# Performance work log

Hardware: AMD Instinct MI355X
Metric: run time of the kernel (lower is better)

The kernel has to match this reference:

```python
import jax, jax.numpy as jnp
import numpy as np

N = 100000
E = 1600000
IN_C = 128
HID = 256
K_EIG = 64
OUT_C = 16


def setup_inputs() -> dict:
    key = jax.random.key(0)
    ks = jax.random.split(key, 8)
    x = jax.random.normal(ks[0], (N, IN_C), dtype=jnp.float32)
    edge_index = jax.random.randint(ks[1], (2, E), 0, N)
    MLP_W = jax.random.normal(ks[2], (K_EIG, N), dtype=jnp.float32) * 0.02
    MLP_b = jax.random.normal(ks[3], (K_EIG,), dtype=jnp.float32) * 0.02
    mlpx_W = jax.random.normal(ks[4], (HID, IN_C), dtype=jnp.float32) * 0.05
    mlpx_b = jax.random.normal(ks[5], (HID,), dtype=jnp.float32) * 0.02
    fin_W = jax.random.normal(ks[6], (OUT_C, HID + K_EIG), dtype=jnp.float32) * 0.05
    fin_b = jax.random.normal(ks[7], (OUT_C,), dtype=jnp.float32) * 0.02
    return {"x": x, "edge_index": edge_index, "MLP_W": MLP_W, "MLP_b": MLP_b,
            "mlpx_W": mlpx_W, "mlpx_b": mlpx_b, "fin_W": fin_W, "fin_b": fin_b}


def _spmm(row, col, feats, n):
    # adj is COO with coords (col[e], row[e]) and value 1 -> out[col] += feats[row]
    return jax.ops.segment_sum(feats[row], col, num_segments=n)


def _pump(xA, row, col, n):
    # MinCut-style pump: soft assignment, normalized-cut loss + orthogonality loss
    S = jax.nn.softmax(xA, axis=-1)                      # [N, K]
    AS = _spmm(row, col, S, n)                            # A @ S, [N, K]
    cut = jnp.sum(S * AS)                                 # tr(S^T A S)
    deg = jax.ops.segment_sum(jnp.ones(col.shape, S.dtype), col, num_segments=n)
    deg_term = jnp.sum(deg[:, None] * S * S)              # tr(S^T D S)
    pump_loss = -(cut / deg_term)
    SS = S.T @ S                                          # [K, K]
    k = S.shape[1]
    ortho_loss = jnp.linalg.norm(SS / jnp.linalg.norm(SS)
                                 - jnp.eye(k, dtype=S.dtype) / jnp.sqrt(jnp.asarray(k, S.dtype)))
    return S, pump_loss, ortho_loss


def reference(x, edge_index, MLP_W, MLP_b, mlpx_W, mlpx_b, fin_W, fin_b):
    row, col = edge_index[0], edge_index[1]
    n = x.shape[0]
    # xA = adj @ MLP.weight.T + bias   (irregular gather/scatter over edges)
    xA = _spmm(row, col, MLP_W.T, n) + MLP_b              # [N, K]
    xX = x @ mlpx_W.T + mlpx_b                            # [N, HID]
    xA, pump_loss, ortho_loss = _pump(xA, row, col, n)
    z = jnp.concatenate([xX, xA], axis=1)                 # [N, HID+K]
    # dropout omitted (eval mode)
    z = jax.nn.log_softmax(z @ fin_W.T + fin_b, axis=-1)  # [N, OUT]
    return (z, pump_loss + ortho_loss)
```

## Files before the change

kernel.cpp:

```cpp
#include <hip/hip_runtime.h>
#include <math.h>

#define N_NODES 100000
#define N_EDGES 1600000
#define IN_C    128
#define HID     256
#define KEIG    64
#define OUT_C   16

#define NPB      256
#define NBUCKET  ((N_NODES + NPB - 1) / NPB)
#define EDGE_TILE 4096
#define NTILE    ((N_EDGES + EDGE_TILE - 1) / EDGE_TILE)
#define CAP      7168

#define TRANS_BLOCKS   ((N_NODES + 63) / 64)
#define GATHER_BLOCKS  2048
#define CUT_BLOCKS     2048
#define SSP_BLOCKS     512
#define OUT_BLOCKS     ((N_NODES + 255) / 256)

typedef __attribute__((ext_vector_type(8))) short short8;
typedef __attribute__((ext_vector_type(4))) float f32x4;

__device__ __forceinline__ float wave_sum(float v) {
#pragma unroll
    for (int m = 32; m; m >>= 1) v += __shfl_xor(v, m, 64);
    return v;
}
__device__ __forceinline__ float wave_max(float v) {
#pragma unroll
    for (int m = 32; m; m >>= 1) v = fmaxf(v, __shfl_xor(v, m, 64));
    return v;
}
__device__ __forceinline__ float bf2f(unsigned int u) {
    return __uint_as_float((u & 0xffffu) << 16);
}
__device__ __forceinline__ unsigned short f2bf(float f) {
    unsigned int u = __float_as_uint(f);
    u += 0x7fff + ((u >> 16) & 1);
    return (unsigned short)(u >> 16);
}
__device__ __forceinline__ float fp8tof(int b) {
    return __builtin_amdgcn_cvt_f32_fp8(b, 0);
}
__device__ __forceinline__ unsigned char f2fp8(float f) {
    int p = __builtin_amdgcn_cvt_pk_fp8_f32(f, f, 0, false);
    return (unsigned char)(p & 0xff);
}

#define FMA4(P, s, W) \
    P.x = fmaf(s, W.x, P.x); P.y = fmaf(s, W.y, P.y); \
    P.z = fmaf(s, W.z, P.z); P.w = fmaf(s, W.w, P.w);

__global__ void prep_weff(const float* __restrict__ mlpxW, const float* __restrict__ mlpxb,
                          const float* __restrict__ finW, const float* __restrict__ finb,
                          float* __restrict__ Weff, float* __restrict__ beff,
                          int* __restrict__ bcnt, unsigned char* __restrict__ WT8,
                          unsigned char* __restrict__ S8, int* __restrict__ gpad) {
    int t = blockIdx.x * blockDim.x + threadIdx.x;
    const int NW = (IN_C + KEIG) * OUT_C;
    if (t < NW) {
        int k = t >> 4, o = t & 15;
        float acc;
        if (k < IN_C) {
            acc = 0.f;
            for (int c = 0; c < HID; ++c)
                acc += mlpxW[c * IN_C + k] * finW[o * (HID + KEIG) + c];
        } else {
            acc = finW[o * (HID + KEIG) + HID + (k - IN_C)];
        }
        Weff[k * OUT_C + o] = acc;
    }
    int tb = t - NW;
    if (tb >= 0 && tb < OUT_C) {
        float acc = finb[tb];
        for (int c = 0; c < HID; ++c) acc += mlpxb[c] * finW[tb * (HID + KEIG) + c];
        beff[tb] = acc;
    }
    int tz = t - (NW + OUT_C);
    if (tz >= 0 && tz <= NBUCKET) bcnt[tz] = 0;
    int tp = t - (NW + OUT_C + NBUCKET + 1);
    if (tp >= 0 && tp < 16) {
        ((int*)(WT8 + (size_t)N_NODES * 64))[tp] = 0;
        ((int*)(S8 + (size_t)N_NODES * 64))[tp] = 0;
        if (tp == 0) *gpad = 0;
    }
}

__global__ void transpose_w(const float* __restrict__ W, unsigned char* __restrict__ WT8) {
    __shared__ float tile[64][65];
    int n0 = blockIdx.x * 64;
    int t = threadIdx.x;
    int tn = t & 63, tq = t >> 6;
#pragma unroll
    for (int kk = 0; kk < 16; ++kk) {
        int k = tq * 16 + kk;
        int n = n0 + tn;
        tile[k][tn] = (n < N_NODES) ? W[(long long)k * N_NODES + n] : 0.f;
    }
    __syncthreads();
    int tk = t & 63;
#pragma unroll
    for (int ii = 0; ii < 16; ++ii) {
        int n = n0 + tq * 16 + ii;
        if (n < N_NODES) WT8[(unsigned)n * 64u + tk] = f2fp8(tile[tk][tq * 16 + ii] * 32.f);
    }
}

__global__ void bucket_hist(const int* __restrict__ ei, int* __restrict__ bcnt) {
    __shared__ int h[NBUCKET];
    int t = threadIdx.x;
    for (int i = t; i < NBUCKET; i += 256) h[i] = 0;
    __syncthreads();
    int e0 = blockIdx.x * EDGE_TILE;
    int e1 = min(e0 + EDGE_TILE, N_EDGES);
    for (int e = e0 + t; e < e1; e += 256)
        atomicAdd(&h[ei[N_EDGES + e] >> 8], 1);
    __syncthreads();
    for (int i = t; i < NBUCKET; i += 256)
        if (h[i]) atomicAdd(&bcnt[i], h[i]);
}

__global__ void bucket_scan(const int* __restrict__ bcnt, int* __restrict__ bbase,
                            int* __restrict__ bcur) {
    __shared__ int sh[512];
    int t = threadIdx.x;
    int v = (t < NBUCKET) ? bcnt[t] : 0;
    sh[t] = v;
    __syncthreads();
    for (int d = 1; d < 512; d <<= 1) {
        int u = (t >= d) ? sh[t - d] : 0;
        __syncthreads();
        sh[t] += u;
        __syncthreads();
    }
    if (t < NBUCKET) { bbase[t] = sh[t] - v; bcur[t] = sh[t] - v; }
    if (t == 0) bbase[NBUCKET] = N_EDGES;
}

__global__ void bucket_scatter(const int* __restrict__ ei, int* __restrict__ bcur,
                               int* __restrict__ ebuf) {
    __shared__ int h[NBUCKET];
    __shared__ int gb[NBUCKET];
    __shared__ int lpre[NBUCKET];
    __shared__ int psum[256];
    __shared__ int stage[EDGE_TILE];
    __shared__ short bkt[EDGE_TILE];
    int t = threadIdx.x;
    for (int i = t; i < NBUCKET; i += 256) h[i] = 0;
    __syncthreads();
    int e0 = blockIdx.x * EDGE_TILE;
    int e1 = min(e0 + EDGE_TILE, N_EDGES);
    int nt = e1 - e0;
    for (int e = e0 + t; e < e1; e += 256)
        atomicAdd(&h[ei[N_EDGES + e] >> 8], 1);
    __syncthreads();
    int a0 = (2 * t < NBUCKET) ? h[2 * t] : 0;
    int a1 = (2 * t + 1 < NBUCKET) ? h[2 * t + 1] : 0;
    psum[t] = a0 + a1;
    __syncthreads();
    for (int d = 1; d < 256; d <<= 1) {
        int u = (t >= d) ? psum[t - d] : 0;
        __syncthreads();
        psum[t] += u;
        __syncthreads();
    }
    int base = (t == 0) ? 0 : psum[t - 1];
    if (2 * t < NBUCKET) lpre[2 * t] = base;
    if (2 * t + 1 < NBUCKET) lpre[2 * t + 1] = base + a0;
    __syncthreads();
    for (int i = t; i < NBUCKET; i += 256) {
        int c = h[i];
        gb[i] = c ? atomicAdd(&bcur[i], c) : 0;
        h[i] = lpre[i];
    }
    __syncthreads();
    for (int e = e0 + t; e < e1; e += 256) {
        int r = ei[e];
        int c = ei[N_EDGES + e];
        int b = c >> 8;
        int slot = atomicAdd(&h[b], 1);
        stage[slot] = r | ((c & 255) << 17);
        bkt[slot] = (short)b;
    }
    __syncthreads();
    for (int s = t; s < nt; s += 256) {
        int b = bkt[s];
        ebuf[gb[b] + s - lpre[b]] = stage[s];
    }
}

__global__ void csr_build(const int* __restrict__ ebuf, const int* __restrict__ bbase,
                          int* __restrict__ offsets, int* __restrict__ pstart,
                          int* __restrict__ csr_row, int* __restrict__ gpad) {
    __shared__ int hist[NPB];
    __shared__ int sh[NPB];
    __shared__ int curs[NPB];
    __shared__ int staged[CAP];
    __shared__ int pbase_sh;
    int b = blockIdx.x;
    int t = threadIdx.x;
    int s0 = bbase[b], s1 = bbase[b + 1];
    hist[t] = 0;
    __syncthreads();
    for (int i = s0 + t; i < s1; i += 256)
        atomicAdd(&hist[ebuf[i] >> 17], 1);
    __syncthreads();
    int v = hist[t];
    int pv = (v + 7) & ~7;
    sh[t] = pv;
    __syncthreads();
    for (int d = 1; d < 256; d <<= 1) {
        int u = (t >= d) ? sh[t - d] : 0;
        __syncthreads();
        sh[t] += u;
        __syncthreads();
    }
    int pexcl = sh[t] - pv;
    int pt = sh[255];
    if (t == 0) pbase_sh = atomicAdd(gpad, pt);
    __syncthreads();
    int pbase = pbase_sh;
    int node = b * NPB + t;
    if (node < N_NODES) { offsets[node] = v; pstart[node] = pbase + pexcl; }
    curs[t] = pexcl;
    __syncthreads();
    if (pt <= CAP) {
        for (int i = t; i < pt; i += 256) staged[i] = N_NODES;
        __syncthreads();
        for (int i = s0 + t; i < s1; i += 256) {
            int pk = ebuf[i];
            int pos = atomicAdd(&curs[pk >> 17], 1);
            staged[pos] = pk & 0x1FFFF;
        }
        __syncthreads();
        for (int i = t; i < pt; i += 256) csr_row[pbase + i] = staged[i];
    } else {
        for (int i = t; i < pt; i += 256) csr_row[pbase + i] = N_NODES;
        __syncthreads();
        for (int i = s0 + t; i < s1; i += 256) {
            int pk = ebuf[i];
            int pos = atomicAdd(&curs[pk >> 17], 1);
            csr_row[pbase + pos] = pk & 0x1FFFF;
        }
    }
}

__global__ void gather_softmax(const int* __restrict__ offsets, const int* __restrict__ pstart,
                               const int* __restrict__ csr_row,
                               const unsigned char* __restrict__ WT8,
                               const float* __restrict__ MLPb,
                               unsigned short* __restrict__ Sb,
                               unsigned char* __restrict__ S8,
                               float* __restrict__ dtp) {
    int lane = threadIdx.x & 63;
    int wib = __builtin_amdgcn_readfirstlane(threadIdx.x >> 6);
    int gw = blockIdx.x * 4 + wib;
    int nw = gridDim.x * 4;
    float bias = MLPb[lane];
    float dacc = 0.f;
    for (int n = gw; n < N_NODES; n += nw) {
        int deg = __builtin_amdgcn_readfirstlane(offsets[n]);
        int ps  = __builtin_amdgcn_readfirstlane(pstart[n]);
        int plen = (deg + 7) & ~7;
        float acc = 0.f;
        for (int j = 0; j < plen; j += 8) {
            int r0 = csr_row[ps + j + 0], r1 = csr_row[ps + j + 1];
            int r2 = csr_row[ps + j + 2], r3 = csr_row[ps + j + 3];
            int r4 = csr_row[ps + j + 4], r5 = csr_row[ps + j + 5];
            int r6 = csr_row[ps + j + 6], r7 = csr_row[ps + j + 7];
            int b0 = WT8[(unsigned)r0 * 64u + lane];
            int b1 = WT8[(unsigned)r1 * 64u + lane];
            int b2 = WT8[(unsigned)r2 * 64u + lane];
            int b3 = WT8[(unsigned)r3 * 64u + lane];
            int b4 = WT8[(unsigned)r4 * 64u + lane];
            int b5 = WT8[(unsigned)r5 * 64u + lane];
            int b6 = WT8[(unsigned)r6 * 64u + lane];
            int b7 = WT8[(unsigned)r7 * 64u + lane];
            acc += ((fp8tof(b0) + fp8tof(b1)) + (fp8tof(b2) + fp8tof(b3)))
                 + ((fp8tof(b4) + fp8tof(b5)) + (fp8tof(b6) + fp8tof(b7)));
        }
        acc = bias + acc * 0.03125f;
        float m = wave_max(acc);
        float e = __expf(acc - m);
        float sm = wave_sum(e);
        float sv = e / sm;
        unsigned idx = (unsigned)n * 64u + lane;
        Sb[idx] = f2bf(sv);
        S8[idx] = f2fp8(sv * 64.f);
        dacc += (float)deg * sv * sv;
    }
    dacc = wave_sum(dacc);
    __shared__ float red[4];
    if (lane == 0) red[wib] = dacc;
    __syncthreads();
    if (threadIdx.x == 0) dtp[blockIdx.x] = red[0] + red[1] + red[2] + red[3];
}

__global__ void cut_csr(const int* __restrict__ offsets, const int* __restrict__ pstart,
                        const int* __restrict__ csr_row,
                        const unsigned short* __restrict__ Sb,
                        const unsigned char* __restrict__ S8, float* __restrict__ cutp) {
    int lane = threadIdx.x & 63;
    int wib = __builtin_amdgcn_readfirstlane(threadIdx.x >> 6);
    int gw = blockIdx.x * 4 + wib;
    int nw = gridDim.x * 4;
    float acc = 0.f;
    for (int n = gw; n < N_NODES; n += nw) {
        float sc = bf2f(Sb[(unsigned)n * 64u + lane]);
        int deg = __builtin_amdgcn_readfirstlane(offsets[n]);
        int ps  = __builtin_amdgcn_readfirstlane(pstart[n]);
        int plen = (deg + 7) & ~7;
        float g = 0.f;
        for (int j = 0; j < plen; j += 8) {
            int r0 = csr_row[ps + j + 0], r1 = csr_row[ps + j + 1];
            int r2 = csr_row[ps + j + 2], r3 = csr_row[ps + j + 3];
            int r4 = csr_row[ps + j + 4], r5 = csr_row[ps + j + 5];
            int r6 = csr_row[ps + j + 6], r7 = csr_row[ps + j + 7];
            int b0 = S8[(unsigned)r0 * 64u + lane];
            int b1 = S8[(unsigned)r1 * 64u + lane];
            int b2 = S8[(unsigned)r2 * 64u + lane];
            int b3 = S8[(unsigned)r3 * 64u + lane];
            int b4 = S8[(unsigned)r4 * 64u + lane];
            int b5 = S8[(unsigned)r5 * 64u + lane];
            int b6 = S8[(unsigned)r6 * 64u + lane];
            int b7 = S8[(unsigned)r7 * 64u + lane];
            g += ((fp8tof(b0) + fp8tof(b1)) + (fp8tof(b2) + fp8tof(b3)))
               + ((fp8tof(b4) + fp8tof(b5)) + (fp8tof(b6) + fp8tof(b7)));
        }
        acc += sc * g * 0.015625f;
    }
    acc = wave_sum(acc);
    __shared__ float red[4];
    if (lane == 0) red[wib] = acc;
    __syncthreads();
    if (threadIdx.x == 0) cutp[blockIdx.x] = red[0] + red[1] + red[2] + red[3];
}

__global__ __launch_bounds__(256) void ss_mfma(const unsigned short* __restrict__ Sb,
                                               float* __restrict__ ssp) {
    __shared__ unsigned short Sr[32][66];
    int t = threadIdx.x;
    int lane = t & 63;
    int w = t >> 6;
    int m = lane & 15;
    int quad = lane >> 4;
    int srow = t >> 3;
    int spart = t & 7;

    f32x4 a0 = {0.f,0.f,0.f,0.f}, a1 = {0.f,0.f,0.f,0.f};
    f32x4 a2 = {0.f,0.f,0.f,0.f}, a3 = {0.f,0.f,0.f,0.f};

    for (int base = blockIdx.x * 32; base < N_NODES; base += SSP_BLOCKS * 32) {
        const uint4* g = (const uint4*)(Sb + (long long)(base + srow) * 64 + spart * 8);
        uint4 d = *g;
        __syncthreads();
        unsigned int* rowp = (unsigned int*)&Sr[srow][0];
        rowp[spart * 4 + 0] = d.x;
        rowp[spart * 4 + 1] = d.y;
        rowp[spart * 4 + 2] = d.z;
        rowp[spart * 4 + 3] = d.w;
        __syncthreads();

        short8 f0, f1, f2, f3;
#pragma unroll
        for (int j = 0; j < 8; ++j) {
            int k = quad * 8 + j;
            f0[j] = (short)Sr[k][m];
            f1[j] = (short)Sr[k][16 + m];
            f2[j] = (short)Sr[k][32 + m];
            f3[j] = (short)Sr[k][48 + m];
        }
        short8 fa = (w == 0) ? f0 : (w == 1) ? f1 : (w == 2) ? f2 : f3;
        a0 = __builtin_amdgcn_mfma_f32_16x16x32_bf16(fa, f0, a0, 0, 0, 0);
        a1 = __builtin_amdgcn_mfma_f32_16x16x32_bf16(fa, f1, a1, 0, 0, 0);
        a2 = __builtin_amdgcn_mfma_f32_16x16x32_bf16(fa, f2, a2, 0, 0, 0);
        a3 = __builtin_amdgcn_mfma_f32_16x16x32_bf16(fa, f3, a3, 0, 0, 0);
    }

    float* dst = ssp + (size_t)blockIdx.x * 4096;
#pragma unroll
    for (int r = 0; r < 4; ++r) {
        int row = w * 16 + quad * 4 + r;
        dst[row * 64 +  0 + m] = a0[r];
        dst[row * 64 + 16 + m] = a1[r];
        dst[row * 64 + 32 + m] = a2[r];
        dst[row * 64 + 48 + m] = a3[r];
    }
}

__global__ void reduce_ss(const float* __restrict__ ssp, float* __restrict__ SS) {
    int e = blockIdx.x * blockDim.x + threadIdx.x;
    float s = 0.f;
    for (int p = 0; p < SSP_BLOCKS; ++p) s += ssp[(size_t)p * 4096 + e];
    SS[e] = s;
}

__global__ void scalars_kernel(const float* __restrict__ cutp, const float* __restrict__ dtp,
                               const float* __restrict__ SS, float* __restrict__ out) {
    __shared__ float red[256];
    int t = threadIdx.x;
    float c = 0.f;
    for (int i = t; i < CUT_BLOCKS; i += 256) c += cutp[i];
    red[t] = c; __syncthreads();
    for (int s = 128; s; s >>= 1) { if (t < s) red[t] += red[t + s]; __syncthreads(); }
    float cut = red[0]; __syncthreads();

    float d = 0.f;
    for (int i = t; i < GATHER_BLOCKS; i += 256) d += dtp[i];
    red[t] = d; __syncthreads();
    for (int s = 128; s; s >>= 1) { if (t < s) red[t] += red[t + s]; __syncthreads(); }
    float dterm = red[0]; __syncthreads();

    float ss[16];
    float sq = 0.f;
#pragma unroll
    for (int j = 0; j < 16; ++j) { ss[j] = SS[t * 16 + j]; sq += ss[j] * ss[j]; }
    red[t] = sq; __syncthreads();
    for (int s = 128; s; s >>= 1) { if (t < s) red[t] += red[t + s]; __syncthreads(); }
    float nrm = sqrtf(red[0]); __syncthreads();

    float osq = 0.f;
#pragma unroll
    for (int j = 0; j < 16; ++j) {
        int idx = t * 16 + j;
        float v = ss[j] / nrm - ((idx % 65 == 0) ? 0.125f : 0.f);
        osq += v * v;
    }
    red[t] = osq; __syncthreads();
    for (int s = 128; s; s >>= 1) { if (t < s) red[t] += red[t + s]; __syncthreads(); }
    if (t == 0) {
        float loss = -(cut / dterm) + sqrtf(red[0]);
        out[(long long)N_NODES * OUT_C] = loss;
    }
}

__global__ __launch_bounds__(256) void out_kernel(const float* __restrict__ x,
                           const unsigned short* __restrict__ Sb,
                           const float* __restrict__ Weff, const float* __restrict__ beff,
                           float* __restrict__ out) {
    __shared__ float4 Wsh[192 * 4];
    __shared__ float bsh[16];
    int t = threadIdx.x;
    const float4* W4 = (const float4*)Weff;
    for (int i = t; i < 768; i += 256) Wsh[i] = W4[i];
    if (t < 16) bsh[t] = beff[t];
    __syncthreads();

    int r = blockIdx.x * 256 + t;
    if (r >= N_NODES) return;

    float4 p0 = make_float4(bsh[0], bsh[1], bsh[2], bsh[3]);
    float4 p1 = make_float4(bsh[4], bsh[5], bsh[6], bsh[7]);
    float4 p2 = make_float4(bsh[8], bsh[9], bsh[10], bsh[11]);
    float4 p3 = make_float4(bsh[12], bsh[13], bsh[14], bsh[15]);

    const float4* xr = (const float4*)(x + (long long)r * IN_C);
#pragma unroll 8
    for (int j = 0; j < 32; ++j) {
        float4 xv = xr[j];
        int k = j * 4;
        float xs[4] = {xv.x, xv.y, xv.z, xv.w};
#pragma unroll
        for (int c = 0; c < 4; ++c) {
            float s = xs[c];
            float4 w0 = Wsh[(k + c) * 4 + 0];
            float4 w1 = Wsh[(k + c) * 4 + 1];
            float4 w2 = Wsh[(k + c) * 4 + 2];
            float4 w3 = Wsh[(k + c) * 4 + 3];
            FMA4(p0, s, w0); FMA4(p1, s, w1); FMA4(p2, s, w2); FMA4(p3, s, w3);
        }
    }
    const uint2* sr = (const uint2*)(Sb + (long long)r * 64);
#pragma unroll 8
    for (int j = 0; j < 16; ++j) {
        uint2 u = sr[j];
        float xs[4] = {bf2f(u.x), bf2f(u.x >> 16), bf2f(u.y), bf2f(u.y >> 16)};
        int k = IN_C + j * 4;
#pragma unroll
        for (int c = 0; c < 4; ++c) {
            float s = xs[c];
            float4 w0 = Wsh[(k + c) * 4 + 0];
            float4 w1 = Wsh[(k + c) * 4 + 1];
            float4 w2 = Wsh[(k + c) * 4 + 2];
            float4 w3 = Wsh[(k + c) * 4 + 3];
            FMA4(p0, s, w0); FMA4(p1, s, w1); FMA4(p2, s, w2); FMA4(p3, s, w3);
        }
    }

    float m = fmaxf(fmaxf(fmaxf(p0.x, p0.y), fmaxf(p0.z, p0.w)),
                    fmaxf(fmaxf(fmaxf(p1.x, p1.y), fmaxf(p1.z, p1.w)),
                          fmaxf(fmaxf(fmaxf(p2.x, p2.y), fmaxf(p2.z, p2.w)),
                                fmaxf(fmaxf(p3.x, p3.y), fmaxf(p3.z, p3.w)))));
    float sum = __expf(p0.x - m) + __expf(p0.y - m) + __expf(p0.z - m) + __expf(p0.w - m)
              + __expf(p1.x - m) + __expf(p1.y - m) + __expf(p1.z - m) + __expf(p1.w - m)
              + __expf(p2.x - m) + __expf(p2.y - m) + __expf(p2.z - m) + __expf(p2.w - m)
              + __expf(p3.x - m) + __expf(p3.y - m) + __expf(p3.z - m) + __expf(p3.w - m);
    float lse = m + logf(sum);
    float4* o4 = (float4*)(out + (long long)r * OUT_C);
    o4[0] = make_float4(p0.x - lse, p0.y - lse, p0.z - lse, p0.w - lse);
    o4[1] = make_float4(p1.x - lse, p1.y - lse, p1.z - lse, p1.w - lse);
    o4[2] = make_float4(p2.x - lse, p2.y - lse, p2.z - lse, p2.w - lse);
    o4[3] = make_float4(p3.x - lse, p3.y - lse, p3.z - lse, p3.w - lse);
}

extern "C" void kernel_launch(void* const* d_in, const int* in_sizes, int n_in,
                              void* d_out, int out_size, void* d_ws, size_t ws_size,
                              hipStream_t stream) {
    const float* x     = (const float*)d_in[0];
    const int*   ei    = (const int*)d_in[1];
    const float* MLPW  = (const float*)d_in[2];
    const float* MLPb  = (const float*)d_in[3];
    const float* mlpxW = (const float*)d_in[4];
    const float* mlpxb = (const float*)d_in[5];
    const float* finW  = (const float*)d_in[6];
    const float* finb  = (const float*)d_in[7];
    float* out = (float*)d_out;
    char* ws = (char*)d_ws;

    unsigned char*  WT8 = (unsigned char*)ws;
    unsigned char*  S8  = (unsigned char*)(ws + (size_t)(N_NODES + 1) * 64);
    unsigned short* Sb  = (unsigned short*)(ws + (size_t)(N_NODES + 1) * 128);
    char* p = ws + (size_t)(N_NODES + 1) * 128 + (size_t)N_NODES * 128;
    float* ssp  = (float*)p;
    float* SS   = ssp + (size_t)SSP_BLOCKS * 4096;
    float* Weff = SS + 4096;
    float* beff = Weff + 192 * 16;
    float* cutp = beff + 16;
    float* dtp  = cutp + CUT_BLOCKS;
    int* ebuf    = (int*)(dtp + GATHER_BLOCKS);
    int* csr_row = ebuf + N_EDGES;
    int* offsets = csr_row + N_EDGES + 8 * ((N_NODES + NPB - 1) / NPB) * NPB + 8 * N_NODES;
    int* pstart  = offsets + N_NODES + 1;
    int* bcnt    = pstart + N_NODES;
    int* bbase   = bcnt + NBUCKET + 1;
    int* bcur    = bbase + NBUCKET + 1;
    int* gpad    = bcur + NBUCKET;

    hipLaunchKernelGGL(prep_weff, dim3(16), dim3(256), 0, stream,
                       mlpxW, mlpxb, finW, finb, Weff, beff, bcnt, WT8, S8, gpad);
    hipLaunchKernelGGL(transpose_w, dim3(TRANS_BLOCKS), dim3(256), 0, stream, MLPW, WT8);
    hipLaunchKernelGGL(bucket_hist, dim3(NTILE), dim3(256), 0, stream, ei, bcnt);
    hipLaunchKernelGGL(bucket_scan, dim3(1), dim3(512), 0, stream, bcnt, bbase, bcur);
    hipLaunchKernelGGL(bucket_scatter, dim3(NTILE), dim3(256), 0, stream, ei, bcur, ebuf);
    hipLaunchKernelGGL(csr_build, dim3(NBUCKET), dim3(256), 0, stream,
                       ebuf, bbase, offsets, pstart, csr_row, gpad);
    hipLaunchKernelGGL(gather_softmax, dim3(GATHER_BLOCKS), dim3(256), 0, stream,
                       offsets, pstart, csr_row, WT8, MLPb, Sb, S8, dtp);
    hipLaunchKernelGGL(cut_csr, dim3(CUT_BLOCKS), dim3(256), 0, stream,
                       offsets, pstart, csr_row, Sb, S8, cutp);
    hipLaunchKernelGGL(ss_mfma, dim3(SSP_BLOCKS), dim3(256), 0, stream, Sb, ssp);
    hipLaunchKernelGGL(reduce_ss, dim3(16), dim3(256), 0, stream, ssp, SS);
    hipLaunchKernelGGL(scalars_kernel, dim3(1), dim3(256), 0, stream, cutp, dtp, SS, out);
    hipLaunchKernelGGL(out_kernel, dim3(OUT_BLOCKS), dim3(256), 0, stream, x, Sb, Weff, beff, out);
}
```

Before: 308.5 us.

## Fuse prep and tail kernels by block range, unroll gathers to 16 edges

Merges transpose_w with bucket_hist into one launch, and cut_csr, ss_mfma and out_kernel into one launch, choosing the branch by block index. The aim is to cut launch gaps and let independent work share the GPU. CSR rows are now padded to multiples of 16 and the gather loops unrolled to 16 loads, for more memory parallelism per wave. In exchange, the padding adds extra dummy reads on low-degree nodes, and a larger CAP raises shared memory per block in csr_build.

```diff
diff --git a/kernel.cpp b/kernel.cpp
--- a/kernel.cpp
+++ b/kernel.cpp
@@ -12,13 +12,14 @@
 #define NBUCKET  ((N_NODES + NPB - 1) / NPB)
 #define EDGE_TILE 4096
 #define NTILE    ((N_EDGES + EDGE_TILE - 1) / EDGE_TILE)
-#define CAP      7168
+#define CAP      8960
 
 #define TRANS_BLOCKS   ((N_NODES + 63) / 64)
 #define GATHER_BLOCKS  2048
 #define CUT_BLOCKS     2048
 #define SSP_BLOCKS     512
 #define OUT_BLOCKS     ((N_NODES + 255) / 256)
+#define TAIL_BLOCKS    (CUT_BLOCKS + SSP_BLOCKS + OUT_BLOCKS)
 
 typedef __attribute__((ext_vector_type(8))) short short8;
 typedef __attribute__((ext_vector_type(4))) float f32x4;
@@ -52,6 +53,29 @@
 #define FMA4(P, s, W) \
     P.x = fmaf(s, W.x, P.x); P.y = fmaf(s, W.y, P.y); \
     P.z = fmaf(s, W.z, P.z); P.w = fmaf(s, W.w, P.w);
+
+#define GATHER16(TBL, DST) do {                                               \
+    int r0 = csr_row[ps + j + 0],  r1 = csr_row[ps + j + 1];                  \
+    int r2 = csr_row[ps + j + 2],  r3 = csr_row[ps + j + 3];                  \
+    int r4 = csr_row[ps + j + 4],  r5 = csr_row[ps + j + 5];                  \
+    int r6 = csr_row[ps + j + 6],  r7 = csr_row[ps + j + 7];                  \
+    int r8 = csr_row[ps + j + 8],  r9 = csr_row[ps + j + 9];                  \
+    int rA = csr_row[ps + j + 10], rB = csr_row[ps + j + 11];                 \
+    int rC = csr_row[ps + j + 12], rD = csr_row[ps + j + 13];                 \
+    int rE = csr_row[ps + j + 14], rF = csr_row[ps + j + 15];                 \
+    int b0 = TBL[(unsigned)r0 * 64u + lane], b1 = TBL[(unsigned)r1 * 64u + lane]; \
+    int b2 = TBL[(unsigned)r2 * 64u + lane], b3 = TBL[(unsigned)r3 * 64u + lane]; \
+    int b4 = TBL[(unsigned)r4 * 64u + lane], b5 = TBL[(unsigned)r5 * 64u + lane]; \
+    int b6 = TBL[(unsigned)r6 * 64u + lane], b7 = TBL[(unsigned)r7 * 64u + lane]; \
+    int b8 = TBL[(unsigned)r8 * 64u + lane], b9 = TBL[(unsigned)r9 * 64u + lane]; \
+    int bA = TBL[(unsigned)rA * 64u + lane], bB = TBL[(unsigned)rB * 64u + lane]; \
+    int bC = TBL[(unsigned)rC * 64u + lane], bD = TBL[(unsigned)rD * 64u + lane]; \
+    int bE = TBL[(unsigned)rE * 64u + lane], bF = TBL[(unsigned)rF * 64u + lane]; \
+    DST += (((fp8tof(b0) + fp8tof(b1)) + (fp8tof(b2) + fp8tof(b3)))           \
+          + ((fp8tof(b4) + fp8tof(b5)) + (fp8tof(b6) + fp8tof(b7))))          \
+         + (((fp8tof(b8) + fp8tof(b9)) + (fp8tof(bA) + fp8tof(bB)))           \
+          + ((fp8tof(bC) + fp8tof(bD)) + (fp8tof(bE) + fp8tof(bF))));         \
+} while (0)
 
 __global__ void prep_weff(const float* __restrict__ mlpxW, const float* __restrict__ mlpxb,
                           const float* __restrict__ finW, const float* __restrict__ finb,
@@ -88,38 +112,42 @@
     }
 }
 
-__global__ void transpose_w(const float* __restrict__ W, unsigned char* __restrict__ WT8) {
-    __shared__ float tile[64][65];
-    int n0 = blockIdx.x * 64;
+__global__ __launch_bounds__(256) void fused_prep(const float* __restrict__ W,
+                                                  unsigned char* __restrict__ WT8,
+                                                  const int* __restrict__ ei,
+                                                  int* __restrict__ bcnt) {
+    __shared__ __align__(16) char sm[64 * 65 * 4];
     int t = threadIdx.x;
-    int tn = t & 63, tq = t >> 6;
-#pragma unroll
-    for (int kk = 0; kk < 16; ++kk) {
-        int k = tq * 16 + kk;
-        int n = n0 + tn;
-        tile[k][tn] = (n < N_NODES) ? W[(long long)k * N_NODES + n] : 0.f;
-    }
-    __syncthreads();
-    int tk = t & 63;
-#pragma unroll
-    for (int ii = 0; ii < 16; ++ii) {
-        int n = n0 + tq * 16 + ii;
-        if (n < N_NODES) WT8[(unsigned)n * 64u + tk] = f2fp8(tile[tk][tq * 16 + ii] * 32.f);
-    }
-}
-
-__global__ void bucket_hist(const int* __restrict__ ei, int* __restrict__ bcnt) {
-    __shared__ int h[NBUCKET];
-    int t = threadIdx.x;
-    for (int i = t; i < NBUCKET; i += 256) h[i] = 0;
-    __syncthreads();
-    int e0 = blockIdx.x * EDGE_TILE;
-    int e1 = min(e0 + EDGE_TILE, N_EDGES);
-    for (int e = e0 + t; e < e1; e += 256)
-        atomicAdd(&h[ei[N_EDGES + e] >> 8], 1);
-    __syncthreads();
-    for (int i = t; i < NBUCKET; i += 256)
-        if (h[i]) atomicAdd(&bcnt[i], h[i]);
+    if (blockIdx.x < TRANS_BLOCKS) {
+        float (*tile)[65] = (float (*)[65])sm;
+        int n0 = blockIdx.x * 64;
+        int tn = t & 63, tq = t >> 6;
+#pragma unroll
+        for (int kk = 0; kk < 16; ++kk) {
+            int k = tq * 16 + kk;
+            int n = n0 + tn;
+            tile[k][tn] = (n < N_NODES) ? W[(long long)k * N_NODES + n] : 0.f;
+        }
+        __syncthreads();
+        int tk = t & 63;
+#pragma unroll
+        for (int ii = 0; ii < 16; ++ii) {
+            int n = n0 + tq * 16 + ii;
+            if (n < N_NODES) WT8[(unsigned)n * 64u + tk] = f2fp8(tile[tk][tq * 16 + ii] * 32.f);
+        }
+    } else {
+        int* h = (int*)sm;
+        for (int i = t; i < NBUCKET; i += 256) h[i] = 0;
+        __syncthreads();
+        int tile_i = blockIdx.x - TRANS_BLOCKS;
+        int e0 = tile_i * EDGE_TILE;
+        int e1 = min(e0 + EDGE_TILE, N_EDGES);
+        for (int e = e0 + t; e < e1; e += 256)
+            atomicAdd(&h[ei[N_EDGES + e] >> 8], 1);
+        __syncthreads();
+        for (int i = t; i < NBUCKET; i += 256)
+            if (h[i]) atomicAdd(&bcnt[i], h[i]);
+    }
 }
 
 __global__ void bucket_scan(const int* __restrict__ bcnt, int* __restrict__ bbase,
@@ -208,7 +236,7 @@
         atomicAdd(&hist[ebuf[i] >> 17], 1);
     __syncthreads();
     int v = hist[t];
-    int pv = (v + 7) & ~7;
+    int pv = (v + 15) & ~15;
     sh[t] = pv;
     __syncthreads();
     for (int d = 1; d < 256; d <<= 1) {
@@ -263,24 +291,9 @@
     for (int n = gw; n < N_NODES; n += nw) {
         int deg = __builtin_amdgcn_readfirstlane(offsets[n]);
         int ps  = __builtin_amdgcn_readfirstlane(pstart[n]);
-        int plen = (deg + 7) & ~7;
+        int plen = (deg + 15) & ~15;
         float acc = 0.f;
-        for (int j = 0; j < plen; j += 8) {
-            int r0 = csr_row[ps + j + 0], r1 = csr_row[ps + j + 1];
-            int r2 = csr_row[ps + j + 2], r3 = csr_row[ps + j + 3];
-            int r4 = csr_row[ps + j + 4], r5 = csr_row[ps + j + 5];
-            int r6 = csr_row[ps + j + 6], r7 = csr_row[ps + j + 7];
-            int b0 = WT8[(unsigned)r0 * 64u + lane];
-            int b1 = WT8[(unsigned)r1 * 64u + lane];
-            int b2 = WT8[(unsigned)r2 * 64u + lane];
-            int b3 = WT8[(unsigned)r3 * 64u + lane];
-            int b4 = WT8[(unsigned)r4 * 64u + lane];
-            int b5 = WT8[(unsigned)r5 * 64u + lane];
-            int b6 = WT8[(unsigned)r6 * 64u + lane];
-            int b7 = WT8[(unsigned)r7 * 64u + lane];
-            acc += ((fp8tof(b0) + fp8tof(b1)) + (fp8tof(b2) + fp8tof(b3)))
-                 + ((fp8tof(b4) + fp8tof(b5)) + (fp8tof(b6) + fp8tof(b7)));
-        }
+        for (int j = 0; j < plen; j += 16) GATHER16(WT8, acc);
         acc = bias + acc * 0.03125f;
         float m = wave_max(acc);
         float e = __expf(acc - m);
@@ -298,95 +311,141 @@
     if (threadIdx.x == 0) dtp[blockIdx.x] = red[0] + red[1] + red[2] + red[3];
 }
 
-__global__ void cut_csr(const int* __restrict__ offsets, const int* __restrict__ pstart,
-                        const int* __restrict__ csr_row,
-                        const unsigned short* __restrict__ Sb,
-                        const unsigned char* __restrict__ S8, float* __restrict__ cutp) {
-    int lane = threadIdx.x & 63;
-    int wib = __builtin_amdgcn_readfirstlane(threadIdx.x >> 6);
-    int gw = blockIdx.x * 4 + wib;
-    int nw = gridDim.x * 4;
-    float acc = 0.f;
-    for (int n = gw; n < N_NODES; n += nw) {
-        float sc = bf2f(Sb[(unsigned)n * 64u + lane]);
-        int deg = __builtin_amdgcn_readfirstlane(offsets[n]);
-        int ps  = __builtin_amdgcn_readfirstlane(pstart[n]);
-        int plen = (deg + 7) & ~7;
-        float g = 0.f;
-        for (int j = 0; j < plen; j += 8) {
-            int r0 = csr_row[ps + j + 0], r1 = csr_row[ps + j + 1];
-            int r2 = csr_row[ps + j + 2], r3 = csr_row[ps + j + 3];
-            int r4 = csr_row[ps + j + 4], r5 = csr_row[ps + j + 5];
-            int r6 = csr_row[ps + j + 6], r7 = csr_row[ps + j + 7];
-            int b0 = S8[(unsigned)r0 * 64u + lane];
-            int b1 = S8[(unsigned)r1 * 64u + lane];
-            int b2 = S8[(unsigned)r2 * 64u + lane];
-            int b3 = S8[(unsigned)r3 * 64u + lane];
-            int b4 = S8[(unsigned)r4 * 64u + lane];
-            int b5 = S8[(unsigned)r5 * 64u + lane];
-            int b6 = S8[(unsigned)r6 * 64u + lane];
-            int b7 = S8[(unsigned)r7 * 64u + lane];
-            g += ((fp8tof(b0) + fp8tof(b1)) + (fp8tof(b2) + fp8tof(b3)))
-               + ((fp8tof(b4) + fp8tof(b5)) + (fp8tof(b6) + fp8tof(b7)));
-        }
-        acc += sc * g * 0.015625f;
-    }
-    acc = wave_sum(acc);
-    __shared__ float red[4];
-    if (lane == 0) red[wib] = acc;
-    __syncthreads();
-    if (threadIdx.x == 0) cutp[blockIdx.x] = red[0] + red[1] + red[2] + red[3];
-}
-
-__global__ __launch_bounds__(256) void ss_mfma(const unsigned short* __restrict__ Sb,
-                                               float* __restrict__ ssp) {
-    __shared__ unsigned short Sr[32][66];
+__global__ __launch_bounds__(256) void fused_tail(
+        const int* __restrict__ offsets, const int* __restrict__ pstart,
+        const int* __restrict__ csr_row,
+        const unsigned short* __restrict__ Sb, const unsigned char* __restrict__ S8,
+        float* __restrict__ cutp, float* __restrict__ ssp,
+        const float* __restrict__ x, const float* __restrict__ Weff,
+        const float* __restrict__ beff, float* __restrict__ out) {
+    __shared__ __align__(16) char sm[768 * 16 + 64];
     int t = threadIdx.x;
-    int lane = t & 63;
-    int w = t >> 6;
-    int m = lane & 15;
-    int quad = lane >> 4;
-    int srow = t >> 3;
-    int spart = t & 7;
-
-    f32x4 a0 = {0.f,0.f,0.f,0.f}, a1 = {0.f,0.f,0.f,0.f};
-    f32x4 a2 = {0.f,0.f,0.f,0.f}, a3 = {0.f,0.f,0.f,0.f};
-
-    for (int base = blockIdx.x * 32; base < N_NODES; base += SSP_BLOCKS * 32) {
-        const uint4* g = (const uint4*)(Sb + (long long)(base + srow) * 64 + spart * 8);
-        uint4 d = *g;
-        __syncthreads();
-        unsigned int* rowp = (unsigned int*)&Sr[srow][0];
-        rowp[spart * 4 + 0] = d.x;
-        rowp[spart * 4 + 1] = d.y;
-        rowp[spart * 4 + 2] = d.z;
-        rowp[spart * 4 + 3] = d.w;
-        __syncthreads();
-
-        short8 f0, f1, f2, f3;
-#pragma unroll
-        for (int j = 0; j < 8; ++j) {
-            int k = quad * 8 + j;
-            f0[j] = (short)Sr[k][m];
-            f1[j] = (short)Sr[k][16 + m];
-            f2[j] = (short)Sr[k][32 + m];
-            f3[j] = (short)Sr[k][48 + m];
-        }
-        short8 fa = (w == 0) ? f0 : (w == 1) ? f1 : (w == 2) ? f2 : f3;
-        a0 = __builtin_amdgcn_mfma_f32_16x16x32_bf16(fa, f0, a0, 0, 0, 0);
-        a1 = __builtin_amdgcn_mfma_f32_16x16x32_bf16(fa, f1, a1, 0, 0, 0);
-        a2 = __builtin_amdgcn_mfma_f32_16x16x32_bf16(fa, f2, a2, 0, 0, 0);
-        a3 = __builtin_amdgcn_mfma_f32_16x16x32_bf16(fa, f3, a3, 0, 0, 0);
-    }
-
-    float* dst = ssp + (size_t)blockIdx.x * 4096;
-#pragma unroll
-    for (int r = 0; r < 4; ++r) {
-        int row = w * 16 + quad * 4 + r;
-        dst[row * 64 +  0 + m] = a0[r];
-        dst[row * 64 + 16 + m] = a1[r];
-        dst[row * 64 + 32 + m] = a2[r];
-        dst[row * 64 + 48 + m] = a3[r];
+    int bid = blockIdx.x;
+
+    if (bid < CUT_BLOCKS) {
+        int lane = t & 63;
+        int wib = __builtin_amdgcn_readfirstlane(t >> 6);
+        int gw = bid * 4 + wib;
+        int nw = CUT_BLOCKS * 4;
+        float acc = 0.f;
+        for (int n = gw; n < N_NODES; n += nw) {
+            float sc = bf2f(Sb[(unsigned)n * 64u + lane]);
+            int deg = __builtin_amdgcn_readfirstlane(offsets[n]);
+            int ps  = __builtin_amdgcn_readfirstlane(pstart[n]);
+            int plen = (deg + 15) & ~15;
+            float g = 0.f;
+            for (int j = 0; j < plen; j += 16) GATHER16(S8, g);
+            acc += sc * g * 0.015625f;
+        }
+        acc = wave_sum(acc);
+        float* red = (float*)sm;
+        if (lane == 0) red[wib] = acc;
+        __syncthreads();
+        if (t == 0) cutp[bid] = red[0] + red[1] + red[2] + red[3];
+    } else if (bid < CUT_BLOCKS + SSP_BLOCKS) {
+        int bid2 = bid - CUT_BLOCKS;
+        unsigned short (*Sr)[66] = (unsigned short (*)[66])sm;
+        int lane = t & 63;
+        int w = t >> 6;
+        int m = lane & 15;
+        int quad = lane >> 4;
+        int srow = t >> 3;
+        int spart = t & 7;
+        f32x4 a0 = {0.f,0.f,0.f,0.f}, a1 = {0.f,0.f,0.f,0.f};
+        f32x4 a2 = {0.f,0.f,0.f,0.f}, a3 = {0.f,0.f,0.f,0.f};
+        for (int base = bid2 * 32; base < N_NODES; base += SSP_BLOCKS * 32) {
+            const uint4* g = (const uint4*)(Sb + (long long)(base + srow) * 64 + spart * 8);
+            uint4 d = *g;
+            __syncthreads();
+            unsigned int* rowp = (unsigned int*)&Sr[srow][0];
+            rowp[spart * 4 + 0] = d.x;
+            rowp[spart * 4 + 1] = d.y;
+            rowp[spart * 4 + 2] = d.z;
+            rowp[spart * 4 + 3] = d.w;
+            __syncthreads();
+            short8 f0, f1, f2, f3;
+#pragma unroll
+            for (int j = 0; j < 8; ++j) {
+                int k = quad * 8 + j;
+                f0[j] = (short)Sr[k][m];
+                f1[j] = (short)Sr[k][16 + m];
+                f2[j] = (short)Sr[k][32 + m];
+                f3[j] = (short)Sr[k][48 + m];
+            }
+            short8 fa = (w == 0) ? f0 : (w == 1) ? f1 : (w == 2) ? f2 : f3;
+            a0 = __builtin_amdgcn_mfma_f32_16x16x32_bf16(fa, f0, a0, 0, 0, 0);
+            a1 = __builtin_amdgcn_mfma_f32_16x16x32_bf16(fa, f1, a1, 0, 0, 0);
+            a2 = __builtin_amdgcn_mfma_f32_16x16x32_bf16(fa, f2, a2, 0, 0, 0);
+            a3 = __builtin_amdgcn_mfma_f32_16x16x32_bf16(fa, f3, a3, 0, 0, 0);
+        }
+        float* dst = ssp + (size_t)bid2 * 4096;
+#pragma unroll
+        for (int r = 0; r < 4; ++r) {
+            int row = w * 16 + quad * 4 + r;
+            dst[row * 64 +  0 + m] = a0[r];
+            dst[row * 64 + 16 + m] = a1[r];
+            dst[row * 64 + 32 + m] = a2[r];
+            dst[row * 64 + 48 + m] = a3[r];
+        }
+    } else {
+        float4* Wsh = (float4*)sm;
+        float* bsh = (float*)(sm + 768 * 16);
+        const float4* W4 = (const float4*)Weff;
+        for (int i = t; i < 768; i += 256) Wsh[i] = W4[i];
+        if (t < 16) bsh[t] = beff[t];
+        __syncthreads();
+        int r = (bid - CUT_BLOCKS - SSP_BLOCKS) * 256 + t;
+        if (r >= N_NODES) return;
+        float4 p0 = make_float4(bsh[0], bsh[1], bsh[2], bsh[3]);
+        float4 p1 = make_float4(bsh[4], bsh[5], bsh[6], bsh[7]);
+        float4 p2 = make_float4(bsh[8], bsh[9], bsh[10], bsh[11]);
+        float4 p3 = make_float4(bsh[12], bsh[13], bsh[14], bsh[15]);
+        const float4* xr = (const float4*)(x + (long long)r * IN_C);
+#pragma unroll 8
+        for (int j = 0; j < 32; ++j) {
+            float4 xv = xr[j];
+            int k = j * 4;
+            float xs[4] = {xv.x, xv.y, xv.z, xv.w};
+#pragma unroll
+            for (int c = 0; c < 4; ++c) {
+                float s = xs[c];
+                float4 w0 = Wsh[(k + c) * 4 + 0];
+                float4 w1 = Wsh[(k + c) * 4 + 1];
+                float4 w2 = Wsh[(k + c) * 4 + 2];
+                float4 w3 = Wsh[(k + c) * 4 + 3];
+                FMA4(p0, s, w0); FMA4(p1, s, w1); FMA4(p2, s, w2); FMA4(p3, s, w3);
+            }
+        }
+        const uint2* sr = (const uint2*)(Sb + (long long)r * 64);
+#pragma unroll 8
+        for (int j = 0; j < 16; ++j) {
+            uint2 u = sr[j];
+            float xs[4] = {bf2f(u.x), bf2f(u.x >> 16), bf2f(u.y), bf2f(u.y >> 16)};
+            int k = IN_C + j * 4;
+#pragma unroll
+            for (int c = 0; c < 4; ++c) {
+                float s = xs[c];
+                float4 w0 = Wsh[(k + c) * 4 + 0];
+                float4 w1 = Wsh[(k + c) * 4 + 1];
+                float4 w2 = Wsh[(k + c) * 4 + 2];
+                float4 w3 = Wsh[(k + c) * 4 + 3];
+                FMA4(p0, s, w0); FMA4(p1, s, w1); FMA4(p2, s, w2); FMA4(p3, s, w3);
+            }
+        }
+        float m = fmaxf(fmaxf(fmaxf(p0.x, p0.y), fmaxf(p0.z, p0.w)),
+                        fmaxf(fmaxf(fmaxf(p1.x, p1.y), fmaxf(p1.z, p1.w)),
+                              fmaxf(fmaxf(fmaxf(p2.x, p2.y), fmaxf(p2.z, p2.w)),
+                                    fmaxf(fmaxf(p3.x, p3.y), fmaxf(p3.z, p3.w)))));
+        float sum = __expf(p0.x - m) + __expf(p0.y - m) + __expf(p0.z - m) + __expf(p0.w - m)
+                  + __expf(p1.x - m) + __expf(p1.y - m) + __expf(p1.z - m) + __expf(p1.w - m)
+                  + __expf(p2.x - m) + __expf(p2.y - m) + __expf(p2.z - m) + __expf(p2.w - m)
+                  + __expf(p3.x - m) + __expf(p3.y - m) + __expf(p3.z - m) + __expf(p3.w - m);
+        float lse = m + logf(sum);
+        float4* o4 = (float4*)(out + (long long)r * OUT_C);
+        o4[0] = make_float4(p0.x - lse, p0.y - lse, p0.z - lse, p0.w - lse);
+        o4[1] = make_float4(p1.x - lse, p1.y - lse, p1.z - lse, p1.w - lse);
+        o4[2] = make_float4(p2.x - lse, p2.y - lse, p2.z - lse, p2.w - lse);
+        o4[3] = make_float4(p3.x - lse, p3.y - lse, p3.z - lse, p3.w - lse);
     }
 }
 
@@ -434,75 +493,6 @@
         float loss = -(cut / dterm) + sqrtf(red[0]);
         out[(long long)N_NODES * OUT_C] = loss;
     }
-}
-
-__global__ __launch_bounds__(256) void out_kernel(const float* __restrict__ x,
-                           const unsigned short* __restrict__ Sb,
-                           const float* __restrict__ Weff, const float* __restrict__ beff,
-                           float* __restrict__ out) {
-    __shared__ float4 Wsh[192 * 4];
-    __shared__ float bsh[16];
-    int t = threadIdx.x;
-    const float4* W4 = (const float4*)Weff;
-    for (int i = t; i < 768; i += 256) Wsh[i] = W4[i];
-    if (t < 16) bsh[t] = beff[t];
-    __syncthreads();
-
-    int r = blockIdx.x * 256 + t;
-    if (r >= N_NODES) return;
-
-    float4 p0 = make_float4(bsh[0], bsh[1], bsh[2], bsh[3]);
-    float4 p1 = make_float4(bsh[4], bsh[5], bsh[6], bsh[7]);
-    float4 p2 = make_float4(bsh[8], bsh[9], bsh[10], bsh[11]);
-    float4 p3 = make_float4(bsh[12], bsh[13], bsh[14], bsh[15]);
-
-    const float4* xr = (const float4*)(x + (long long)r * IN_C);
-#pragma unroll 8
-    for (int j = 0; j < 32; ++j) {
-        float4 xv = xr[j];
-        int k = j * 4;
-        float xs[4] = {xv.x, xv.y, xv.z, xv.w};
-#pragma unroll
-        for (int c = 0; c < 4; ++c) {
-            float s = xs[c];
-            float4 w0 = Wsh[(k + c) * 4 + 0];
-            float4 w1 = Wsh[(k + c) * 4 + 1];
-            float4 w2 = Wsh[(k + c) * 4 + 2];
-            float4 w3 = Wsh[(k + c) * 4 + 3];
-            FMA4(p0, s, w0); FMA4(p1, s, w1); FMA4(p2, s, w2); FMA4(p3, s, w3);
-        }
-    }
-    const uint2* sr = (const uint2*)(Sb + (long long)r * 64);
-#pragma unroll 8
-    for (int j = 0; j < 16; ++j) {
-        uint2 u = sr[j];
-        float xs[4] = {bf2f(u.x), bf2f(u.x >> 16), bf2f(u.y), bf2f(u.y >> 16)};
-        int k = IN_C + j * 4;
-#pragma unroll
-        for (int c = 0; c < 4; ++c) {
-            float s = xs[c];
-            float4 w0 = Wsh[(k + c) * 4 + 0];
-            float4 w1 = Wsh[(k + c) * 4 + 1];
-            float4 w2 = Wsh[(k + c) * 4 + 2];
-            float4 w3 = Wsh[(k + c) * 4 + 3];
-            FMA4(p0, s, w0); FMA4(p1, s, w1); FMA4(p2, s, w2); FMA4(p3, s, w3);
-        }
-    }
-
-    float m = fmaxf(fmaxf(fmaxf(p0.x, p0.y), fmaxf(p0.z, p0.w)),
-                    fmaxf(fmaxf(fmaxf(p1.x, p1.y), fmaxf(p1.z, p1.w)),
-                          fmaxf(fmaxf(fmaxf(p2.x, p2.y), fmaxf(p2.z, p2.w)),
-                                fmaxf(fmaxf(p3.x, p3.y), fmaxf(p3.z, p3.w)))));
-    float sum = __expf(p0.x - m) + __expf(p0.y - m) + __expf(p0.z - m) + __expf(p0.w - m)
-              + __expf(p1.x - m) + __expf(p1.y - m) + __expf(p1.z - m) + __expf(p1.w - m)
-              + __expf(p2.x - m) + __expf(p2.y - m) + __expf(p2.z - m) + __expf(p2.w - m)
-              + __expf(p3.x - m) + __expf(p3.y - m) + __expf(p3.z - m) + __expf(p3.w - m);
-    float lse = m + logf(sum);
-    float4* o4 = (float4*)(out + (long long)r * OUT_C);
-    o4[0] = make_float4(p0.x - lse, p0.y - lse, p0.z - lse, p0.w - lse);
-    o4[1] = make_float4(p1.x - lse, p1.y - lse, p1.z - lse, p1.w - lse);
-    o4[2] = make_float4(p2.x - lse, p2.y - lse, p2.z - lse, p2.w - lse);
-    o4[3] = make_float4(p3.x - lse, p3.y - lse, p3.z - lse, p3.w - lse);
 }
 
 extern "C" void kernel_launch(void* const* d_in, const int* in_sizes, int n_in,
@@ -531,7 +521,7 @@
     float* dtp  = cutp + CUT_BLOCKS;
     int* ebuf    = (int*)(dtp + GATHER_BLOCKS);
     int* csr_row = ebuf + N_EDGES;
-    int* offsets = csr_row + N_EDGES + 8 * ((N_NODES + NPB - 1) / NPB) * NPB + 8 * N_NODES;
+    int* offsets = csr_row + N_EDGES + 16 * N_NODES;
     int* pstart  = offsets + N_NODES + 1;
     int* bcnt    = pstart + N_NODES;
     int* bbase   = bcnt + NBUCKET + 1;
@@ -540,18 +530,16 @@
 
     hipLaunchKernelGGL(prep_weff, dim3(16), dim3(256), 0, stream,
                        mlpxW, mlpxb, finW, finb, Weff, beff, bcnt, WT8, S8, gpad);
-    hipLaunchKernelGGL(transpose_w, dim3(TRANS_BLOCKS), dim3(256), 0, stream, MLPW, WT8);
-    hipLaunchKernelGGL(bucket_hist, dim3(NTILE), dim3(256), 0, stream, ei, bcnt);
+    hipLaunchKernelGGL(fused_prep, dim3(TRANS_BLOCKS + NTILE), dim3(256), 0, stream,
+                       MLPW, WT8, ei, bcnt);
     hipLaunchKernelGGL(bucket_scan, dim3(1), dim3(512), 0, stream, bcnt, bbase, bcur);
     hipLaunchKernelGGL(bucket_scatter, dim3(NTILE), dim3(256), 0, stream, ei, bcur, ebuf);
     hipLaunchKernelGGL(csr_build, dim3(NBUCKET), dim3(256), 0, stream,
                        ebuf, bbase, offsets, pstart, csr_row, gpad);
     hipLaunchKernelGGL(gather_softmax, dim3(GATHER_BLOCKS), dim3(256), 0, stream,
                        offsets, pstart, csr_row, WT8, MLPb, Sb, S8, dtp);
-    hipLaunchKernelGGL(cut_csr, dim3(CUT_BLOCKS), dim3(256), 0, stream,
-                       offsets, pstart, csr_row, Sb, S8, cutp);
-    hipLaunchKernelGGL(ss_mfma, dim3(SSP_BLOCKS), dim3(256), 0, stream, Sb, ssp);
+    hipLaunchKernelGGL(fused_tail, dim3(TAIL_BLOCKS), dim3(256), 0, stream,
+                       offsets, pstart, csr_row, Sb, S8, cutp, ssp, x, Weff, beff, out);
     hipLaunchKernelGGL(reduce_ss, dim3(16), dim3(256), 0, stream, ssp, SS);
     hipLaunchKernelGGL(scalars_kernel, dim3(1), dim3(256), 0, stream, cutp, dtp, SS, out);
-    hipLaunchKernelGGL(out_kernel, dim3(OUT_BLOCKS), dim3(256), 0, stream, x, Sb, Weff, beff, out);
-}
+}
```

Measured after the change: 310.1 us. About the same (+0.5%).
